# Kernel tuning notes

Measured on AMD Instinct MI355X. Metric: run time of the kernel, lower is better.

The kernel has to match this reference:

```python
import jax, jax.numpy as jnp
import numpy as np

POOL = 7  # adaptive_avg_pool2d output size (7,7)


def _bin_edges(start, length):
    """Adaptive-avg-pool bin boundaries.
    start, length: [N] int32 -> (lo, hi) each [N, POOL] absolute indices,
    matching torch: lo_i = floor(i*L/P), hi_i = ceil((i+1)*L/P).
    """
    i = jnp.arange(POOL, dtype=jnp.int32)
    lo = start[:, None] + (i[None, :] * length[:, None]) // POOL
    hi = start[:, None] + (-((-(i[None, :] + 1)) * length[:, None] // POOL))
    # note: ceil(a/b) = -(-a // b); written below explicitly
    hi = start[:, None] - ((-(i[None, :] + 1) * length[:, None]) // POOL)
    return lo, hi


def roi_adaptive_avg_pool(features, rois):
    """features: [1, C, H, W]; rois: [N, 4] int (x1,y1,x2,y2 inclusive).
    Returns [N, C, POOL, POOL] == torch stack of adaptive_avg_pool2d over
    features[:, :, y1:y2+1, x1:x2+1], vectorized via an integral image.
    """
    B, C, H, W = features.shape  # B == 1 (forced by shared_fcs input dim)
    # integral image with a zero row/col prepended: ii[y, x] = sum over [:y, :x]
    ii = jnp.cumsum(jnp.cumsum(features, axis=2), axis=3)
    ii = jnp.pad(ii, ((0, 0), (0, 0), (1, 0), (1, 0)))[0]  # [C, H+1, W+1]

    x1, y1, x2, y2 = rois[:, 0], rois[:, 1], rois[:, 2], rois[:, 3]
    ys, ye = _bin_edges(y1, y2 - y1 + 1)   # [N, POOL]
    xs, xe = _bin_edges(x1, x2 - x1 + 1)
    Y0, Y1 = ys[:, :, None], ye[:, :, None]   # [N, POOL, 1]
    X0, X1 = xs[:, None, :], xe[:, None, :]   # [N, 1, POOL]

    def gather(Y, X):
        return ii[:, Y, X]  # [C, N, POOL, POOL]

    sums = gather(Y1, X1) - gather(Y0, X1) - gather(Y1, X0) + gather(Y0, X0)
    area = ((Y1 - Y0) * (X1 - X0)).astype(features.dtype)  # [N, POOL, POOL]
    pooled = sums / area[None]                              # [C, N, POOL, POOL]
    return jnp.transpose(pooled, (1, 0, 2, 3))              # [N, C, POOL, POOL]


def setup_inputs() -> dict:
    key = jax.random.key(0)
    ks = jax.random.split(key, 12)
    C, H, W, N, F = 256, 336, 336, 2000, 256
    features = jax.random.normal(ks[0], (1, C, H, W), dtype=jnp.float32)
    # valid small ROIs (shuttlecock-sized), x1<=x2, y1<=y2, in-bounds
    x1 = jax.random.randint(ks[1], (N,), 0, W - 40)
    y1 = jax.random.randint(ks[2], (N,), 0, H - 40)
    bw = jax.random.randint(ks[3], (N,), 4, 40)
    bh = jax.random.randint(ks[4], (N,), 4, 40)
    rois = jnp.stack([x1, y1, jnp.minimum(x1 + bw, W - 1),
                      jnp.minimum(y1 + bh, H - 1)], axis=1).astype(jnp.int32)
    d_in = C * POOL * POOL
    w1 = jax.random.normal(ks[5], (d_in, F), dtype=jnp.float32) * (1.0 / np.sqrt(d_in))
    b1 = jnp.zeros((F,), dtype=jnp.float32)
    w2 = jax.random.normal(ks[6], (F, F), dtype=jnp.float32) * (1.0 / np.sqrt(F))
    b2 = jnp.zeros((F,), dtype=jnp.float32)
    w_cls = jax.random.normal(ks[7], (F, 2), dtype=jnp.float32) * 0.01
    b_cls = jnp.zeros((2,), dtype=jnp.float32)
    w_reg = jax.random.normal(ks[8], (F, 4), dtype=jnp.float32) * 0.001
    b_reg = jnp.zeros((4,), dtype=jnp.float32)
    return {"features": features, "rois": rois, "w1": w1, "b1": b1,
            "w2": w2, "b2": b2, "w_cls": w_cls, "b_cls": b_cls,
            "w_reg": w_reg, "b_reg": b_reg}


def reference(features, rois, w1, b1, w2, b2, w_cls, b_cls, w_reg, b_reg):
    roi_feats = roi_adaptive_avg_pool(features, rois)          # [N, C, 7, 7]
    roi_feats = roi_feats.reshape(roi_feats.shape[0], -1)      # [N, C*49]
    h = jax.nn.relu(roi_feats @ w1 + b1)
    h = jax.nn.relu(h @ w2 + b2)
    cls_score = h @ w_cls + b_cls                              # [N, num_classes+1]
    bbox_pred = h @ w_reg + b_reg                              # [N, 4]
    return (cls_score, bbox_pred)
```

## Files before the change

kernel.cpp:

```cpp
#include <hip/hip_runtime.h>

typedef unsigned int uint;
typedef unsigned short ushort;
typedef __bf16 v8bf __attribute__((ext_vector_type(8)));
typedef float v4f __attribute__((ext_vector_type(4)));

#define CCH 256
#define HH 336
#define WW 336
#define HWSZ (HH*WW)
#define NROI 2000
#define KDIM 12544
#define MPAD 2048
#define SPLITK 14
#define KSP (KDIM/SPLITK)

__device__ __forceinline__ ushort bf16r(float f) {
  uint u = __float_as_uint(f);
  u += 0x7fffu + ((u >> 16) & 1u);
  return (ushort)(u >> 16);
}
__device__ __forceinline__ uint packbf(float a, float b) {
  return (uint)bf16r(a) | ((uint)bf16r(b) << 16);
}

typedef const __attribute__((address_space(1))) uint* gas_t;
typedef __attribute__((address_space(3))) uint* las_t;
__device__ __forceinline__ void async16(const void* g, void* l) {
  __builtin_amdgcn_global_load_lds((gas_t)g, (las_t)l, 16, 0, 0);
}

__global__ __launch_bounds__(256) void k_transpose(const float* __restrict__ f,
                                                   uint* __restrict__ ftu) {
  __shared__ uint T[64 * 134];
  int tid = threadIdx.x;
  int hw0 = blockIdx.x * 64;
  int hwl = tid & 63;
  int cq = tid >> 6;
  int hw = hw0 + hwl;
#pragma unroll 4
  for (int it = 0; it < 32; ++it) {
    int c = it * 8 + cq * 2;
    float a = f[(size_t)c * HWSZ + hw];
    float b = f[(size_t)(c + 1) * HWSZ + hw];
    T[hwl * 134 + it * 4 + cq] = packbf(a, b);
  }
  __syncthreads();
  int co = tid & 31, r = tid >> 5;
#pragma unroll
  for (int i = 0; i < 8; ++i) {
    int hwr = i * 8 + r;
    uint2 v0 = *(const uint2*)&T[hwr * 134 + co * 4];
    uint2 v1 = *(const uint2*)&T[hwr * 134 + co * 4 + 2];
    *(uint4*)(ftu + (size_t)(hw0 + hwr) * 128 + co * 4) =
        make_uint4(v0.x, v0.y, v1.x, v1.y);
  }
}

__global__ __launch_bounds__(256) void k_w1perm(const float* __restrict__ w1,
                                                uint* __restrict__ w1t_u) {
  int bin = blockIdx.x % 49;
  int c0 = (blockIdx.x / 49) * 32;
  __shared__ ushort T[32][258];
  int n = threadIdx.x;
  for (int i = 0; i < 32; ++i)
    T[i][n] = bf16r(w1[(size_t)((c0 + i) * 49 + bin) * 256 + n]);
  __syncthreads();
  int cc = threadIdx.x & 15;
  int nb = threadIdx.x >> 4;
  for (int rep = 0; rep < 16; ++rep) {
    int nn = rep * 16 + nb;
    uint v = (uint)T[2 * cc][nn] | ((uint)T[2 * cc + 1][nn] << 16);
    w1t_u[(size_t)nn * (KDIM / 2) + bin * 128 + c0 / 2 + cc] = v;
  }
}

__global__ __launch_bounds__(256) void k_w2t(const float* __restrict__ w2,
                                             ushort* __restrict__ w2t) {
  int n = blockIdx.x, k = threadIdx.x;
  w2t[n * 256 + k] = bf16r(w2[k * 256 + n]);
}

__global__ __launch_bounds__(256) void k_sort(const int* __restrict__ rois,
                                              int* __restrict__ perm) {
  __shared__ int hist[64];
  __shared__ int keys[NROI];
  int tid = threadIdx.x;
  if (tid < 64) hist[tid] = 0;
  __syncthreads();
  for (int i = tid; i < NROI; i += 256) {
    int x1 = rois[i * 4 + 0], y1 = rois[i * 4 + 1];
    int x2 = rois[i * 4 + 2], y2 = rois[i * 4 + 3];
    int cx = (x1 + x2) >> 1, cy = (y1 + y2) >> 1;
    int k = (cy / 42) * 8 + (cx / 42);
    keys[i] = k;
    atomicAdd(&hist[k], 1);
  }
  __syncthreads();
  if (tid < 64) {
    int v = hist[tid];
    int s = v;
#pragma unroll
    for (int d = 1; d < 64; d <<= 1) {
      int t = __shfl_up(s, d, 64);
      if (tid >= d) s += t;
    }
    hist[tid] = s - v;
  }
  __syncthreads();
  for (int i = tid; i < NROI; i += 256) {
    int pos = atomicAdd(&hist[keys[i]], 1);
    perm[pos] = i;
  }
}

#define UNPK8(A, u) do {                                     \
  A[0] += __uint_as_float((u).x << 16);                      \
  A[1] += __uint_as_float((u).x & 0xffff0000u);              \
  A[2] += __uint_as_float((u).y << 16);                      \
  A[3] += __uint_as_float((u).y & 0xffff0000u);              \
  A[4] += __uint_as_float((u).z << 16);                      \
  A[5] += __uint_as_float((u).z & 0xffff0000u);              \
  A[6] += __uint_as_float((u).w << 16);                      \
  A[7] += __uint_as_float((u).w & 0xffff0000u);              \
} while (0)

__global__ __launch_bounds__(64) void k_pool(const int* __restrict__ rois,
                                             const int* __restrict__ perm,
                                             const uint4* __restrict__ ft4,
                                             uint4* __restrict__ rf4) {
  int L = blockIdx.x;
  int i = L >> 3;
  int slot = (L & 7) * 250 + i / 7;
  int by = i % 7;
  int n = perm[slot];
  int t = threadIdx.x;
  int co = t & 31, par = t >> 5;
  int x1 = rois[n * 4 + 0], y1 = rois[n * 4 + 1];
  int x2 = rois[n * 4 + 2], y2 = rois[n * 4 + 3];
  int Lw = x2 - x1 + 1, Lh = y2 - y1 + 1;
  int ylo = y1 + (by * Lh) / 7;
  int yhi = y1 + ((by + 1) * Lh + 6) / 7;
  int rh = yhi - ylo;
  uint ob = (uint)n * 1568 + (uint)by * 224 + co;
  for (int b = 0; b < 7; ++b) {
    int lo = x1 + (b * Lw) / 7;
    int hi = x1 + ((b + 1) * Lw + 6) / 7;
    float a[8], c[8];
#pragma unroll
    for (int j = 0; j < 8; ++j) { a[j] = 0.f; c[j] = 0.f; }
    for (int y = ylo; y < yhi; ++y) {
      const uint4* p = ft4 + (size_t)(y * WW + lo + par) * 32 + co;
      int x = lo + par;
      for (; x + 2 < hi; x += 4) {
        uint4 u0 = p[0], u1 = p[64];
        p += 128;
        UNPK8(a, u0);
        UNPK8(c, u1);
      }
      for (; x < hi; x += 2) {
        uint4 u = p[0];
        p += 64;
        UNPK8(a, u);
      }
    }
#pragma unroll
    for (int j = 0; j < 8; ++j) a[j] += c[j];
#pragma unroll
    for (int j = 0; j < 8; ++j) a[j] += __shfl_xor(a[j], 32, 64);
    if (t < 32) {
      float inv = 1.0f / (float)(rh * (hi - lo));
      uint4 o;
      o.x = packbf(a[0] * inv, a[1] * inv);
      o.y = packbf(a[2] * inv, a[3] * inv);
      o.z = packbf(a[4] * inv, a[5] * inv);
      o.w = packbf(a[6] * inv, a[7] * inv);
      rf4[ob + b * 32] = o;
    }
  }
}

__global__ __launch_bounds__(256) void k_gemm1(const ushort* __restrict__ A,
                                               const ushort* __restrict__ B,
                                               float* __restrict__ P) {
  __shared__ ushort As[64 * 64];
  __shared__ ushort Bs[128 * 64];
  int m0 = blockIdx.x * 64;
  int n0 = blockIdx.y * 128;
  int ks = blockIdx.z;
  int k0 = ks * KSP;
  int tid = threadIdx.x;
  int lane = tid & 63, wv = tid >> 6;
  int wm = wv & 1, wn = wv >> 1;
  int lm = lane & 15, quad = lane >> 4;
  int srow = tid >> 3, scol = (tid & 7) * 8;
  v4f acc[2][4];
#pragma unroll
  for (int i = 0; i < 2; ++i)
#pragma unroll
    for (int j = 0; j < 4; ++j) acc[i][j] = (v4f){0.f, 0.f, 0.f, 0.f};
  const ushort* Ab = A + (size_t)(m0 + srow) * KDIM + k0 + scol;
  const ushort* Bb = B + (size_t)(n0 + srow) * KDIM + k0 + scol;
  for (int kt = 0; kt < KSP / 64; ++kt) {
    __syncthreads();
#pragma unroll
    for (int r = 0; r < 2; ++r)
      async16(Ab + (size_t)(r * 32) * KDIM + kt * 64, &As[(srow + r * 32) * 64 + scol]);
#pragma unroll
    for (int r = 0; r < 4; ++r)
      async16(Bb + (size_t)(r * 32) * KDIM + kt * 64, &Bs[(srow + r * 32) * 64 + scol]);
    __syncthreads();
#pragma unroll
    for (int kk = 0; kk < 64; kk += 32) {
      v8bf a[2], b[4];
#pragma unroll
      for (int i = 0; i < 2; ++i)
        a[i] = *(const v8bf*)&As[(wm * 32 + i * 16 + lm) * 64 + kk + quad * 8];
#pragma unroll
      for (int j = 0; j < 4; ++j)
        b[j] = *(const v8bf*)&Bs[(wn * 64 + j * 16 + lm) * 64 + kk + quad * 8];
#pragma unroll
      for (int i = 0; i < 2; ++i)
#pragma unroll
        for (int j = 0; j < 4; ++j)
          acc[i][j] = __builtin_amdgcn_mfma_f32_16x16x32_bf16(a[i], b[j], acc[i][j], 0, 0, 0);
    }
  }
  float* Pb = P + (size_t)ks * MPAD * 256;
#pragma unroll
  for (int i = 0; i < 2; ++i)
#pragma unroll
    for (int j = 0; j < 4; ++j) {
      int row = m0 + wm * 32 + i * 16 + quad * 4;
      int col = n0 + wn * 64 + j * 16 + lm;
#pragma unroll
      for (int r = 0; r < 4; ++r)
        Pb[(size_t)(row + r) * 256 + col] = acc[i][j][r];
    }
}

__global__ __launch_bounds__(256) void k_reduce(const float* __restrict__ P,
                                                const float* __restrict__ b1,
                                                uint* __restrict__ h1u) {
  int idx = blockIdx.x * 256 + threadIdx.x;
  int m = idx >> 7, np = idx & 127;
  const float2* Pp = (const float2*)P;
  float2 s = {0.f, 0.f};
#pragma unroll
  for (int ks = 0; ks < SPLITK; ++ks) {
    float2 v = Pp[(size_t)(ks * MPAD + m) * 128 + np];
    s.x += v.x; s.y += v.y;
  }
  s.x += b1[2 * np]; s.y += b1[2 * np + 1];
  s.x = fmaxf(s.x, 0.f); s.y = fmaxf(s.y, 0.f);
  h1u[idx] = packbf(s.x, s.y);
}

__global__ __launch_bounds__(256) void k_gemm2(const ushort* __restrict__ h1b,
                                               const ushort* __restrict__ w2t,
                                               const float* __restrict__ b2,
                                               const float* __restrict__ wcls,
                                               const float* __restrict__ bcls,
                                               const float* __restrict__ wreg,
                                               const float* __restrict__ breg,
                                               float* __restrict__ out) {
  __shared__ ushort As2[64 * 64];
  __shared__ ushort Bs2[256 * 64];
  __shared__ float Hs[64 * 257];
  int tid = threadIdx.x;
  int r0 = blockIdx.x * 64;
  int lane = tid & 63, wv = tid >> 6;
  int lm = lane & 15, quad = lane >> 4;
  int srow = tid >> 3, scol = (tid & 7) * 8;
  v4f acc[16];
#pragma unroll
  for (int j = 0; j < 16; ++j) acc[j] = (v4f){0.f, 0.f, 0.f, 0.f};
  for (int kt = 0; kt < 4; ++kt) {
    __syncthreads();
#pragma unroll
    for (int r = 0; r < 2; ++r)
      async16(h1b + (size_t)(r0 + srow + r * 32) * 256 + kt * 64 + scol,
              &As2[(srow + r * 32) * 64 + scol]);
#pragma unroll
    for (int r = 0; r < 8; ++r)
      async16(w2t + (size_t)(srow + r * 32) * 256 + kt * 64 + scol,
              &Bs2[(srow + r * 32) * 64 + scol]);
    __syncthreads();
#pragma unroll
    for (int kk = 0; kk < 64; kk += 32) {
      v8bf a = *(const v8bf*)&As2[(wv * 16 + lm) * 64 + kk + quad * 8];
#pragma unroll
      for (int j = 0; j < 16; ++j) {
        v8bf b = *(const v8bf*)&Bs2[(j * 16 + lm) * 64 + kk + quad * 8];
        acc[j] = __builtin_amdgcn_mfma_f32_16x16x32_bf16(a, b, acc[j], 0, 0, 0);
      }
    }
  }
#pragma unroll
  for (int j = 0; j < 16; ++j) {
    int nn = j * 16 + lm;
    float bb = b2[nn];
#pragma unroll
    for (int r = 0; r < 4; ++r) {
      int row = wv * 16 + quad * 4 + r;
      Hs[row * 257 + nn] = fmaxf(acc[j][r] + bb, 0.f);
    }
  }
  __syncthreads();
  for (int o = tid; o < 384; o += 256) {
    int hd = o >> 6, r = o & 63;
    int grow = r0 + r;
    float d = 0.f;
    if (hd < 2) {
      for (int k = 0; k < 256; ++k) d += Hs[r * 257 + k] * wcls[k * 2 + hd];
      d += bcls[hd];
      if (grow < NROI) out[grow * 2 + hd] = d;
    } else {
      int h4 = hd - 2;
      for (int k = 0; k < 256; ++k) d += Hs[r * 257 + k] * wreg[k * 4 + h4];
      d += breg[h4];
      if (grow < NROI) out[4000 + grow * 4 + h4] = d;
    }
  }
}

extern "C" void kernel_launch(void* const* d_in, const int* in_sizes, int n_in,
                              void* d_out, int out_size, void* d_ws, size_t ws_size,
                              hipStream_t stream) {
  const float* features = (const float*)d_in[0];
  const int* rois = (const int*)d_in[1];
  const float* w1 = (const float*)d_in[2];
  const float* b1 = (const float*)d_in[3];
  const float* w2 = (const float*)d_in[4];
  const float* b2 = (const float*)d_in[5];
  const float* wcls = (const float*)d_in[6];
  const float* bcls = (const float*)d_in[7];
  const float* wreg = (const float*)d_in[8];
  const float* breg = (const float*)d_in[9];
  char* ws = (char*)d_ws;
  ushort* ft  = (ushort*)(ws + 0);
  ushort* w1t = (ushort*)(ws + 57802752);
  ushort* w2t = (ushort*)(ws + 64225280);
  ushort* rf  = (ushort*)(ws + 64356352);
  int*    perm = (int*)(ws + 64356352 + (size_t)NROI * KDIM * 2);
  float*  P   = (float*)(ws + 115736576);
  ushort* h1b = (ushort*)(ws + 145096704);
  float* out = (float*)d_out;

  hipLaunchKernelGGL(k_transpose, dim3(HWSZ / 64), dim3(256), 0, stream,
                     features, (uint*)ft);
  hipLaunchKernelGGL(k_w1perm, dim3(392), dim3(256), 0, stream, w1, (uint*)w1t);
  hipLaunchKernelGGL(k_w2t, dim3(256), dim3(256), 0, stream, w2, w2t);
  hipLaunchKernelGGL(k_sort, dim3(1), dim3(256), 0, stream, rois, perm);
  hipLaunchKernelGGL(k_pool, dim3(NROI * 7), dim3(64), 0, stream, rois, perm,
                     (const uint4*)ft, (uint4*)rf);
  hipLaunchKernelGGL(k_gemm1, dim3(32, 2, SPLITK), dim3(256), 0, stream, rf, w1t, P);
  hipLaunchKernelGGL(k_reduce, dim3(1024), dim3(256), 0, stream, P, b1, (uint*)h1b);
  hipLaunchKernelGGL(k_gemm2, dim3(32), dim3(256), 0, stream, h1b, w2t, b2, wcls, bcls, wreg, breg, out);
}
```

Baseline: 353.1 us.

## Vectorize feature transpose, merge prep kernels, unroll pooling over row pairs

The feature transpose now loads float4 per channel and handles 128 spatial positions per block, giving wider global loads and half as many blocks. The w1 permute, w2 transpose and ROI sort kernels are merged into one launch, which cuts launch overhead and lets the single-block sort run alongside the other work. The pooling loop walks two rows per iteration with four accumulator sets, so more independent loads are in flight. In exchange, the transpose uses twice the LDS per block and pooling uses more registers, which can lower occupancy.

```diff
diff --git a/kernel.cpp b/kernel.cpp
--- a/kernel.cpp
+++ b/kernel.cpp
@@ -32,85 +32,92 @@
 
 __global__ __launch_bounds__(256) void k_transpose(const float* __restrict__ f,
                                                    uint* __restrict__ ftu) {
-  __shared__ uint T[64 * 134];
+  __shared__ uint T[128 * 134];
   int tid = threadIdx.x;
-  int hw0 = blockIdx.x * 64;
-  int hwl = tid & 63;
-  int cq = tid >> 6;
-  int hw = hw0 + hwl;
-#pragma unroll 4
-  for (int it = 0; it < 32; ++it) {
-    int c = it * 8 + cq * 2;
-    float a = f[(size_t)c * HWSZ + hw];
-    float b = f[(size_t)(c + 1) * HWSZ + hw];
-    T[hwl * 134 + it * 4 + cq] = packbf(a, b);
+  int hw0 = blockIdx.x * 128;
+  int hwq = tid & 31;
+  int cp = tid >> 5;
+#pragma unroll 2
+  for (int j = 0; j < 16; ++j) {
+    int cpair = j * 8 + cp;
+    int c = cpair * 2;
+    float4 fa = *(const float4*)&f[(size_t)c * HWSZ + hw0 + hwq * 4];
+    float4 fb = *(const float4*)&f[(size_t)(c + 1) * HWSZ + hw0 + hwq * 4];
+    T[(hwq * 4 + 0) * 134 + cpair] = packbf(fa.x, fb.x);
+    T[(hwq * 4 + 1) * 134 + cpair] = packbf(fa.y, fb.y);
+    T[(hwq * 4 + 2) * 134 + cpair] = packbf(fa.z, fb.z);
+    T[(hwq * 4 + 3) * 134 + cpair] = packbf(fa.w, fb.w);
   }
   __syncthreads();
   int co = tid & 31, r = tid >> 5;
-#pragma unroll
-  for (int i = 0; i < 8; ++i) {
-    int hwr = i * 8 + r;
-    uint2 v0 = *(const uint2*)&T[hwr * 134 + co * 4];
-    uint2 v1 = *(const uint2*)&T[hwr * 134 + co * 4 + 2];
-    *(uint4*)(ftu + (size_t)(hw0 + hwr) * 128 + co * 4) =
+#pragma unroll 4
+  for (int i = 0; i < 16; ++i) {
+    int row = i * 8 + r;
+    uint2 v0 = *(const uint2*)&T[row * 134 + co * 4];
+    uint2 v1 = *(const uint2*)&T[row * 134 + co * 4 + 2];
+    *(uint4*)(ftu + (size_t)(hw0 + row) * 128 + co * 4) =
         make_uint4(v0.x, v0.y, v1.x, v1.y);
   }
 }
 
-__global__ __launch_bounds__(256) void k_w1perm(const float* __restrict__ w1,
-                                                uint* __restrict__ w1t_u) {
-  int bin = blockIdx.x % 49;
-  int c0 = (blockIdx.x / 49) * 32;
+__global__ __launch_bounds__(256) void k_prep(const float* __restrict__ w1,
+                                              uint* __restrict__ w1t_u,
+                                              const float* __restrict__ w2,
+                                              ushort* __restrict__ w2t,
+                                              const int* __restrict__ rois,
+                                              int* __restrict__ perm) {
   __shared__ ushort T[32][258];
-  int n = threadIdx.x;
-  for (int i = 0; i < 32; ++i)
-    T[i][n] = bf16r(w1[(size_t)((c0 + i) * 49 + bin) * 256 + n]);
-  __syncthreads();
-  int cc = threadIdx.x & 15;
-  int nb = threadIdx.x >> 4;
-  for (int rep = 0; rep < 16; ++rep) {
-    int nn = rep * 16 + nb;
-    uint v = (uint)T[2 * cc][nn] | ((uint)T[2 * cc + 1][nn] << 16);
-    w1t_u[(size_t)nn * (KDIM / 2) + bin * 128 + c0 / 2 + cc] = v;
-  }
-}
-
-__global__ __launch_bounds__(256) void k_w2t(const float* __restrict__ w2,
-                                             ushort* __restrict__ w2t) {
-  int n = blockIdx.x, k = threadIdx.x;
-  w2t[n * 256 + k] = bf16r(w2[k * 256 + n]);
-}
-
-__global__ __launch_bounds__(256) void k_sort(const int* __restrict__ rois,
-                                              int* __restrict__ perm) {
   __shared__ int hist[64];
   __shared__ int keys[NROI];
   int tid = threadIdx.x;
-  if (tid < 64) hist[tid] = 0;
-  __syncthreads();
-  for (int i = tid; i < NROI; i += 256) {
-    int x1 = rois[i * 4 + 0], y1 = rois[i * 4 + 1];
-    int x2 = rois[i * 4 + 2], y2 = rois[i * 4 + 3];
-    int cx = (x1 + x2) >> 1, cy = (y1 + y2) >> 1;
-    int k = (cy / 42) * 8 + (cx / 42);
-    keys[i] = k;
-    atomicAdd(&hist[k], 1);
-  }
-  __syncthreads();
-  if (tid < 64) {
-    int v = hist[tid];
-    int s = v;
-#pragma unroll
-    for (int d = 1; d < 64; d <<= 1) {
-      int t = __shfl_up(s, d, 64);
-      if (tid >= d) s += t;
-    }
-    hist[tid] = s - v;
-  }
-  __syncthreads();
-  for (int i = tid; i < NROI; i += 256) {
-    int pos = atomicAdd(&hist[keys[i]], 1);
-    perm[pos] = i;
+  int b = blockIdx.x;
+  if (b < 392) {
+    int bin = b % 49;
+    int c0 = (b / 49) * 32;
+    int n = tid;
+    for (int i = 0; i < 32; ++i)
+      T[i][n] = bf16r(w1[(size_t)((c0 + i) * 49 + bin) * 256 + n]);
+    __syncthreads();
+    int cc = tid & 15;
+    int nb = tid >> 4;
+    for (int rep = 0; rep < 16; ++rep) {
+      int nn = rep * 16 + nb;
+      uint v = (uint)T[2 * cc][nn] | ((uint)T[2 * cc + 1][nn] << 16);
+      w1t_u[(size_t)nn * (KDIM / 2) + bin * 128 + c0 / 2 + cc] = v;
+    }
+  } else if (b < 424) {
+    int n = (b - 392) * 8 + (tid >> 5);
+    for (int kl = 0; kl < 8; ++kl) {
+      int k = kl * 32 + (tid & 31);
+      w2t[n * 256 + k] = bf16r(w2[k * 256 + n]);
+    }
+  } else {
+    if (tid < 64) hist[tid] = 0;
+    __syncthreads();
+    for (int i = tid; i < NROI; i += 256) {
+      int x1 = rois[i * 4 + 0], y1 = rois[i * 4 + 1];
+      int x2 = rois[i * 4 + 2], y2 = rois[i * 4 + 3];
+      int cx = (x1 + x2) >> 1, cy = (y1 + y2) >> 1;
+      int k = (cy / 42) * 8 + (cx / 42);
+      keys[i] = k;
+      atomicAdd(&hist[k], 1);
+    }
+    __syncthreads();
+    if (tid < 64) {
+      int v = hist[tid];
+      int s = v;
+#pragma unroll
+      for (int d = 1; d < 64; d <<= 1) {
+        int t2 = __shfl_up(s, d, 64);
+        if (tid >= d) s += t2;
+      }
+      hist[tid] = s - v;
+    }
+    __syncthreads();
+    for (int i = tid; i < NROI; i += 256) {
+      int pos = atomicAdd(&hist[keys[i]], 1);
+      perm[pos] = i;
+    }
   }
 }
 
@@ -146,10 +153,31 @@
   for (int b = 0; b < 7; ++b) {
     int lo = x1 + (b * Lw) / 7;
     int hi = x1 + ((b + 1) * Lw + 6) / 7;
-    float a[8], c[8];
-#pragma unroll
-    for (int j = 0; j < 8; ++j) { a[j] = 0.f; c[j] = 0.f; }
-    for (int y = ylo; y < yhi; ++y) {
+    float a[8], c[8], d[8], e[8];
+#pragma unroll
+    for (int j = 0; j < 8; ++j) { a[j] = 0.f; c[j] = 0.f; d[j] = 0.f; e[j] = 0.f; }
+    int y = ylo;
+    for (; y + 1 < yhi; y += 2) {
+      const uint4* p = ft4 + (size_t)(y * WW + lo + par) * 32 + co;
+      const uint4* q = p + 336 * 32;
+      int x = lo + par;
+      for (; x + 2 < hi; x += 4) {
+        uint4 u0 = p[0], u1 = p[64];
+        uint4 v0 = q[0], v1 = q[64];
+        p += 128; q += 128;
+        UNPK8(a, u0);
+        UNPK8(c, u1);
+        UNPK8(d, v0);
+        UNPK8(e, v1);
+      }
+      for (; x < hi; x += 2) {
+        uint4 u = p[0], v = q[0];
+        p += 64; q += 64;
+        UNPK8(a, u);
+        UNPK8(d, v);
+      }
+    }
+    if (y < yhi) {
       const uint4* p = ft4 + (size_t)(y * WW + lo + par) * 32 + co;
       int x = lo + par;
       for (; x + 2 < hi; x += 4) {
@@ -165,7 +193,7 @@
       }
     }
 #pragma unroll
-    for (int j = 0; j < 8; ++j) a[j] += c[j];
+    for (int j = 0; j < 8; ++j) a[j] += c[j] + d[j] + e[j];
 #pragma unroll
     for (int j = 0; j < 8; ++j) a[j] += __shfl_xor(a[j], 32, 64);
     if (t < 32) {
@@ -347,11 +375,10 @@
   ushort* h1b = (ushort*)(ws + 145096704);
   float* out = (float*)d_out;
 
-  hipLaunchKernelGGL(k_transpose, dim3(HWSZ / 64), dim3(256), 0, stream,
+  hipLaunchKernelGGL(k_transpose, dim3(HWSZ / 128), dim3(256), 0, stream,
                      features, (uint*)ft);
-  hipLaunchKernelGGL(k_w1perm, dim3(392), dim3(256), 0, stream, w1, (uint*)w1t);
-  hipLaunchKernelGGL(k_w2t, dim3(256), dim3(256), 0, stream, w2, w2t);
-  hipLaunchKernelGGL(k_sort, dim3(1), dim3(256), 0, stream, rois, perm);
+  hipLaunchKernelGGL(k_prep, dim3(425), dim3(256), 0, stream,
+                     w1, (uint*)w1t, w2, w2t, rois, perm);
   hipLaunchKernelGGL(k_pool, dim3(NROI * 7), dim3(64), 0, stream, rois, perm,
                      (const uint4*)ft, (uint4*)rf);
   hipLaunchKernelGGL(k_gemm1, dim3(32, 2, SPLITK), dim3(256), 0, stream, rf, w1t, P);
```

New measurement: 351.3 us. About the same (-0.5%).
